# Performance work log

Hardware: AMD Instinct MI355X
Metric: run time of the kernel (lower is better)

Reference implementation:

```python
import jax, jax.numpy as jnp
import numpy as np

N, E = 10000, 100000
WIDTH, KER_WIDTH, DEPTH = 32, 128, 3
EDGE_ATTR_DIM, IN_WIDTH, OUT_WIDTH, COORD_DIM = 6, 3, 1, 3


def _glorot(k, fan_in, fan_out):
    return jax.random.normal(k, (fan_in, fan_out), jnp.float32) / np.sqrt(fan_in).astype(np.float32)


def setup_inputs() -> dict:
    key = jax.random.key(0)
    ks = jax.random.split(key, 16)
    z = lambda n: jnp.zeros((n,), jnp.float32)
    return {
        "x": jax.random.normal(ks[0], (N, IN_WIDTH), jnp.float32),
        "edge_index": jax.random.randint(ks[1], (2, E), 0, N),
        "edge_attr": jax.random.normal(ks[2], (E, EDGE_ATTR_DIM), jnp.float32),
        "coords_init": jax.random.normal(ks[3], (N, COORD_DIM), jnp.float32),
        "fc1_w": _glorot(ks[4], IN_WIDTH, WIDTH), "fc1_b": z(WIDTH),
        "ker_w1": _glorot(ks[5], EDGE_ATTR_DIM + 1, KER_WIDTH // 2), "ker_b1": z(KER_WIDTH // 2),
        "ker_w2": _glorot(ks[6], KER_WIDTH // 2, KER_WIDTH), "ker_b2": z(KER_WIDTH),
        "ker_w3": _glorot(ks[7], KER_WIDTH, WIDTH * WIDTH), "ker_b3": z(WIDTH * WIDTH),
        "cm_w1": _glorot(ks[8], WIDTH, WIDTH), "cm_b1": z(WIDTH),
        "cm_w2": _glorot(ks[9], WIDTH, 1) * 1e-3,  # xavier gain=0.001 coord head, no bias
        "fc2_w1": _glorot(ks[10], WIDTH, 2 * WIDTH), "fc2_b1": z(2 * WIDTH),
        "fc2_w2": _glorot(ks[11], 2 * WIDTH, OUT_WIDTH), "fc2_b2": z(OUT_WIDTH),
    }


def _seg_mean(data, seg, n):
    s = jax.ops.segment_sum(data, seg, num_segments=n)
    c = jax.ops.segment_sum(jnp.ones((seg.shape[0], 1), data.dtype), seg, num_segments=n)
    return s / jnp.clip(c, 1.0)


def reference(x, edge_index, edge_attr, coords_init,
              fc1_w, fc1_b, ker_w1, ker_b1, ker_w2, ker_b2, ker_w3, ker_b3,
              cm_w1, cm_b1, cm_w2, fc2_w1, fc2_b1, fc2_w2, fc2_b2):
    row, col = edge_index[0], edge_index[1]
    h = x @ fc1_w + fc1_b                                   # [N, W]
    coord = coords_init
    for _ in range(DEPTH):
        coord_diff = coord[row] - coord[col]                # [E, 3]
        radial = jnp.sum(coord_diff * coord_diff, axis=-1, keepdims=True)
        kin = jnp.concatenate([edge_attr, radial], axis=-1)  # [E, ker_in]
        k = jax.nn.relu(kin @ ker_w1 + ker_b1)
        k = jax.nn.relu(k @ ker_w2 + ker_b2)
        Wk = (k @ ker_w3 + ker_b3).reshape(E, WIDTH, WIDTH)  # per-edge kernel matrix
        m = jnp.einsum('eij,ej->ei', Wk, h[col])             # per-edge message [E, W]
        phi = jax.nn.relu(m @ cm_w1 + cm_b1) @ cm_w2         # [E, 1]
        coord = coord + _seg_mean(coord_diff * phi, row, N)  # equivariant coord update
        h = jax.nn.relu(h + _seg_mean(m, row, N))            # GKN node update
    out = jax.nn.relu(h @ fc2_w1 + fc2_b1) @ fc2_w2 + fc2_b2  # [N, out_width]
    return out, coord
```

## Files before the change

kernel.cpp:

```cpp
#include <hip/hip_runtime.h>
#include <hip/hip_bf16.h>

#define NN 10000
#define NE 100000

typedef __bf16 bf16x8 __attribute__((ext_vector_type(8)));
typedef float  f32x4  __attribute__((ext_vector_type(4)));
typedef unsigned int u32x4 __attribute__((ext_vector_type(4)));

__device__ __forceinline__ f32x4 relu4(f32x4 a) {
    a.x = fmaxf(a.x, 0.f); a.y = fmaxf(a.y, 0.f);
    a.z = fmaxf(a.z, 0.f); a.w = fmaxf(a.w, 0.f);
    return a;
}


__global__ void k_setup(const float* __restrict__ w3, __bf16* __restrict__ w3sw,
                        const float* __restrict__ w2, __bf16* __restrict__ w2sw,
                        const float* __restrict__ x, const float* __restrict__ fc1w,
                        const float* __restrict__ fc1b, const float* __restrict__ cinit,
                        float* __restrict__ h, float* __restrict__ coord,
                        const int* __restrict__ eidx, int* __restrict__ deg,
                        int* __restrict__ within) {
    int t = blockIdx.x * blockDim.x + threadIdx.x;
    if (t < 131072) {
        int jj = t & 7;
        int L  = (t >> 3) & 63;
        int ks = (t >> 9) & 3;
        int jt = (t >> 11) & 1;
        int i  = t >> 12;
        int c    = ks*32 + (L >> 4)*8 + jj;
        int colv = i*32 + jt*16 + (L & 15);
        w3sw[t] = (__bf16)w3[c*1024 + colv];
    } else if (t < 139264) {
        int u = t - 131072;
        int jj = u & 7;
        int L  = (u >> 3) & 63;
        int ks = (u >> 9) & 1;
        int nt = u >> 10;
        int c1 = ks*32 + (L >> 4)*8 + jj;
        int c2 = nt*16 + (L & 15);
        w2sw[u] = (__bf16)w2[c1*128 + c2];
    } else if (t < 139264 + NN) {
        int n = t - 139264;
        float x0 = x[n*3+0], x1 = x[n*3+1], x2 = x[n*3+2];
        #pragma unroll
        for (int j = 0; j < 32; j += 4) {
            f32x4 a = *(const f32x4*)(fc1b + j);
            a += x0 * (*(const f32x4*)(fc1w + 0*32 + j));
            a += x1 * (*(const f32x4*)(fc1w + 1*32 + j));
            a += x2 * (*(const f32x4*)(fc1w + 2*32 + j));
            *(f32x4*)(h + n*32 + j) = a;
        }
        coord[n*3+0] = cinit[n*3+0];
        coord[n*3+1] = cinit[n*3+1];
        coord[n*3+2] = cinit[n*3+2];
    } else if (t < 139264 + NN + NE) {
        int e = t - 139264 - NN;
        within[e] = atomicAdd(&deg[eidx[e]], 1);
    }
}

__global__ __launch_bounds__(1024, 1)
void k_scan(const int* __restrict__ deg, int* __restrict__ rowptr,
            float* __restrict__ deg_inv) {
    __shared__ int ssum[1024];
    const int tid = threadIdx.x;
    const int CH = 10;
    const int base = tid * CH;
    int s = 0;
    for (int i = 0; i < CH; ++i) { int n = base + i; if (n < NN) s += deg[n]; }
    ssum[tid] = s;
    __syncthreads();
    for (int off = 1; off < 1024; off <<= 1) {
        int t = (tid >= off) ? ssum[tid - off] : 0;
        __syncthreads();
        ssum[tid] += t;
        __syncthreads();
    }
    int run = ssum[tid] - s;
    for (int i = 0; i < CH; ++i) {
        int n = base + i;
        if (n < NN) {
            int d = deg[n];
            rowptr[n] = run; run += d;
            deg_inv[n] = 1.0f / (float)(d > 1 ? d : 1);
        }
    }
    if (tid == 1023) rowptr[NN] = ssum[1023];
}

__global__ __launch_bounds__(256, 2)
void k_layer(const float* __restrict__ coord, const int* __restrict__ eidx,
             const float* __restrict__ eattr,
             const float* __restrict__ w1, const float* __restrict__ b1,
             const __bf16* __restrict__ w2sw, const float* __restrict__ b2,
             const __bf16* __restrict__ w3sw, const float* __restrict__ b3,
             const float* __restrict__ h,
             const float* __restrict__ cm_w1, const float* __restrict__ cm_b1,
             const float* __restrict__ cm_w2,
             const int* __restrict__ rowptr, const int* __restrict__ within,
             float* __restrict__ cds, float* __restrict__ m_s,
             float* __restrict__ phis) {
    __shared__ unsigned smem_u[6656];
    __bf16* kt1 = (__bf16*)smem_u;
    __bf16* kt2 = (__bf16*)smem_u + 5120;
    const int lane = threadIdx.x & 63;
    const int wave = threadIdx.x >> 6;
    const int q = lane >> 4, t = lane & 15;
    const int base = blockIdx.x * 64;

    const int eg = base + lane;
    const int egc = eg < NE ? eg : NE - 1;
    const bool wvalid = eg < NE;
    const int r_node = eidx[egc];
    const int pos = rowptr[r_node] + within[egc];

    int col = eidx[NE + egc];
    float hcol[32];
    {
        const f32x4* hp = (const f32x4*)(h + (size_t)col * 32);
        #pragma unroll
        for (int v = 0; v < 8; ++v) {
            f32x4 hv = hp[v];
            hcol[v*4+0] = hv.x; hcol[v*4+1] = hv.y; hcol[v*4+2] = hv.z; hcol[v*4+3] = hv.w;
        }
    }
    bf16x8 bcur[8];
    {
        const __bf16* wb0 = w3sw + (size_t)(wave * 8) * 4096;
        #pragma unroll
        for (int f = 0; f < 8; ++f)
            bcur[f] = *(const bf16x8*)(wb0 + (f*64 + lane) * 8);
    }

    {
        float dx = coord[r_node*3+0] - coord[col*3+0];
        float dy = coord[r_node*3+1] - coord[col*3+1];
        float dz = coord[r_node*3+2] - coord[col*3+2];
        float rad = dx*dx + dy*dy + dz*dz;
        if (wave == 0 && wvalid) {
            f32x4 cdv = {dx, dy, dz, rad};
            *(f32x4*)(cds + (size_t)pos*4) = cdv;
        }
        float kin[7];
        #pragma unroll
        for (int a = 0; a < 6; ++a) kin[a] = eattr[(size_t)egc*6 + a];
        kin[6] = rad;

        const int g0 = wave * 16;
        f32x4 acc1[4];
        #pragma unroll
        for (int g = 0; g < 4; ++g) acc1[g] = *(const f32x4*)(b1 + g0 + g*4);
        #pragma unroll
        for (int t7 = 0; t7 < 7; ++t7) {
            float kv = kin[t7];
            #pragma unroll
            for (int g = 0; g < 4; ++g)
                acc1[g] += kv * (*(const f32x4*)(w1 + t7*64 + g0 + g*4));
        }
        #pragma unroll
        for (int cc = 0; cc < 2; ++cc) {
            f32x4 a0 = relu4(acc1[cc*2]), a1 = relu4(acc1[cc*2+1]);
            bf16x8 pk = {(__bf16)a0.x, (__bf16)a0.y, (__bf16)a0.z, (__bf16)a0.w,
                         (__bf16)a1.x, (__bf16)a1.y, (__bf16)a1.z, (__bf16)a1.w};
            int chunk = wave*2 + cc;
            *(bf16x8*)(kt1 + lane*72 + ((chunk ^ (lane & 7)) * 8)) = pk;
        }
    }
    __syncthreads();

    {
        bf16x8 af[4][2];
        #pragma unroll
        for (int mt = 0; mt < 4; ++mt) {
            int ep = mt*16 + t;
            #pragma unroll
            for (int ks = 0; ks < 2; ++ks)
                af[mt][ks] = *(const bf16x8*)(kt1 + ep*72 + (((ks*4 + q) ^ (ep & 7)) * 8));
        }
        #pragma unroll
        for (int nn = 0; nn < 2; ++nn) {
            int nt = wave*2 + nn;
            f32x4 a2[4];
            #pragma unroll
            for (int mt = 0; mt < 4; ++mt) a2[mt] = (f32x4){0.f, 0.f, 0.f, 0.f};
            #pragma unroll
            for (int ks = 0; ks < 2; ++ks) {
                bf16x8 bf_ = *(const bf16x8*)(w2sw + ((nt*2 + ks)*64 + lane) * 8);
                #pragma unroll
                for (int mt = 0; mt < 4; ++mt)
                    a2[mt] = __builtin_amdgcn_mfma_f32_16x16x32_bf16(af[mt][ks], bf_, a2[mt], 0, 0, 0);
            }
            float bias = b2[nt*16 + t];
            int chunk = nt*2 + (t >> 3);
            int tin = t & 7;
            #pragma unroll
            for (int mt = 0; mt < 4; ++mt) {
                #pragma unroll
                for (int rr = 0; rr < 4; ++rr) {
                    int row = mt*16 + q*4 + rr;
                    kt2[row*128 + ((chunk ^ (row & 15)) * 8) + tin] =
                        (__bf16)fmaxf(a2[mt][rr] + bias, 0.f);
                }
            }
        }
    }
    __syncthreads();

    bf16x8 afrag[4][4];
    #pragma unroll
    for (int mt = 0; mt < 4; ++mt) {
        int ep = mt*16 + t;
        #pragma unroll
        for (int ks = 0; ks < 4; ++ks) {
            int ck = ks*4 + q;
            afrag[mt][ks] = *(const bf16x8*)(kt2 + ep*128 + ((ck ^ (ep & 15)) * 8));
        }
    }
    __syncthreads();

    unsigned* wkw = smem_u + wave * 1280;
    const unsigned* wkrow = wkw + lane * 20;
    const int maskr = (lane ^ (lane >> 3)) & 3;
    float mv[8];

    #pragma unroll
    for (int ii = 0; ii < 8; ++ii) {
        const int i = wave * 8 + ii;
        f32x4 acc[4][2];
        #pragma unroll
        for (int mt = 0; mt < 4; ++mt) {
            acc[mt][0] = (f32x4){0.f, 0.f, 0.f, 0.f};
            acc[mt][1] = (f32x4){0.f, 0.f, 0.f, 0.f};
        }
        #pragma unroll
        for (int jt = 0; jt < 2; ++jt) {
            #pragma unroll
            for (int ks = 0; ks < 4; ++ks) {
                bf16x8 bfrag = bcur[jt*4 + ks];
                #pragma unroll
                for (int mt = 0; mt < 4; ++mt)
                    acc[mt][jt] = __builtin_amdgcn_mfma_f32_16x16x32_bf16(
                        afrag[mt][ks], bfrag, acc[mt][jt], 0, 0, 0);
            }
        }
        if (ii < 7) {
            const __bf16* wbn = w3sw + (size_t)(i + 1) * 4096;
            #pragma unroll
            for (int f = 0; f < 8; ++f)
                bcur[f] = *(const bf16x8*)(wbn + (f*64 + lane) * 8);
        }
        float bias0 = b3[i*32 + t];
        float bias1 = b3[i*32 + 16 + t];
        #pragma unroll
        for (int mt = 0; mt < 4; ++mt) {
            #pragma unroll
            for (int r = 0; r < 4; ++r) {
                int row = mt*16 + q*4 + r;
                float a0 = acc[mt][0][r] + bias0;
                float a1 = acc[mt][1][r] + bias1;
                unsigned u0 = (unsigned)__builtin_bit_cast(unsigned short, (__bf16)a0);
                unsigned u1 = (unsigned)__builtin_bit_cast(unsigned short, (__bf16)a1);
                int msk = (row ^ (row >> 3)) & 3;
                wkw[row*20 + ((((t >> 2) ^ msk) << 2) | (t & 3))] = u0 | (u1 << 16);
            }
        }
        float s = 0.f;
        #pragma unroll
        for (int j = 0; j < 4; ++j) {
            u32x4 wv = *(const u32x4*)(wkrow + ((j ^ maskr) << 2));
            #pragma unroll
            for (int k = 0; k < 4; ++k) {
                unsigned w = wv[k];
                int c = j*4 + k;
                float flo = __uint_as_float(w << 16);
                float fhi = __uint_as_float(w & 0xFFFF0000u);
                s += flo * hcol[c] + fhi * hcol[16 + c];
            }
        }
        mv[ii] = s;
    }

    if (wvalid) {
        f32x4 v0 = {mv[0], mv[1], mv[2], mv[3]};
        f32x4 v1 = {mv[4], mv[5], mv[6], mv[7]};
        *(f32x4*)(m_s + (size_t)pos*32 + wave*8)     = v0;
        *(f32x4*)(m_s + (size_t)pos*32 + wave*8 + 4) = v1;
    }

    __syncthreads();
    float* mvx = (float*)smem_u;
    #pragma unroll
    for (int ii = 0; ii < 8; ++ii)
        mvx[(wave*8 + ii)*65 + lane] = mv[ii];
    __syncthreads();
    if (wave == 0) {
        float m2[32];
        #pragma unroll
        for (int i = 0; i < 32; ++i) m2[i] = mvx[i*65 + lane];
        float phi = 0.f;
        for (int o = 0; o < 32; o += 4) {
            f32x4 a = *(const f32x4*)(cm_b1 + o);
            #pragma unroll
            for (int i = 0; i < 32; ++i)
                a += m2[i] * (*(const f32x4*)(cm_w1 + i*32 + o));
            a = relu4(a);
            f32x4 w2 = *(const f32x4*)(cm_w2 + o);
            phi += a.x*w2.x + a.y*w2.y + a.z*w2.z + a.w*w2.w;
        }
        if (wvalid) phis[pos] = phi;
    }
}

__global__ __launch_bounds__(256, 4)
void k_gather(const int* __restrict__ rowptr,
              const float* __restrict__ m_s, const float* __restrict__ phis,
              const float* __restrict__ cds, const float* __restrict__ deg_inv,
              float* __restrict__ coord, float* __restrict__ h,
              const float* __restrict__ fw1, const float* __restrict__ fb1,
              const float* __restrict__ fw2, const float* __restrict__ fb2,
              float* __restrict__ out, int dofinal) {
    int tid = blockIdx.x * blockDim.x + threadIdx.x;
    int n = tid >> 3, sub = tid & 7;
    if (n >= NN) return;
    int st = rowptr[n], en = rowptr[n+1];
    f32x4 am0 = {0.f, 0.f, 0.f, 0.f}, am1 = {0.f, 0.f, 0.f, 0.f};
    int p = st;
    for (; p + 1 < en; p += 2) {
        am0 += *(const f32x4*)(m_s + (size_t)p*32 + sub*4);
        am1 += *(const f32x4*)(m_s + (size_t)(p+1)*32 + sub*4);
    }
    if (p < en) am0 += *(const f32x4*)(m_s + (size_t)p*32 + sub*4);
    f32x4 am = am0 + am1;

    float di = deg_inv[n];
    f32x4 hv = *(const f32x4*)(h + (size_t)n*32 + sub*4);
    hv = relu4(hv + am * di);

    float c0 = 0.f, c1 = 0.f, c2 = 0.f;
    if (sub == 0) {
        float cx0 = 0.f, cy0 = 0.f, cz0 = 0.f;
        float cx1 = 0.f, cy1 = 0.f, cz1 = 0.f;
        int pp = st;
        for (; pp + 1 < en; pp += 2) {
            f32x4 cd0 = *(const f32x4*)(cds + (size_t)pp*4);
            f32x4 cd1 = *(const f32x4*)(cds + (size_t)(pp+1)*4);
            float p0 = phis[pp], p1 = phis[pp+1];
            cx0 += cd0.x * p0; cy0 += cd0.y * p0; cz0 += cd0.z * p0;
            cx1 += cd1.x * p1; cy1 += cd1.y * p1; cz1 += cd1.z * p1;
        }
        if (pp < en) {
            f32x4 cd0 = *(const f32x4*)(cds + (size_t)pp*4);
            float p0 = phis[pp];
            cx0 += cd0.x * p0; cy0 += cd0.y * p0; cz0 += cd0.z * p0;
        }
        c0 = coord[n*3+0] + (cx0 + cx1) * di;
        c1 = coord[n*3+1] + (cy0 + cy1) * di;
        c2 = coord[n*3+2] + (cz0 + cz1) * di;
    }

    if (!dofinal) {
        *(f32x4*)(h + (size_t)n*32 + sub*4) = hv;
        if (sub == 0) {
            coord[n*3+0] = c0; coord[n*3+1] = c1; coord[n*3+2] = c2;
        }
        return;
    }

    const int gbase = (tid & 63) & 56;
    float hreg[32];
    #pragma unroll
    for (int s2 = 0; s2 < 8; ++s2) {
        hreg[s2*4+0] = __shfl(hv.x, gbase + s2, 64);
        hreg[s2*4+1] = __shfl(hv.y, gbase + s2, 64);
        hreg[s2*4+2] = __shfl(hv.z, gbase + s2, 64);
        hreg[s2*4+3] = __shfl(hv.w, gbase + s2, 64);
    }
    float po = 0.f;
    #pragma unroll
    for (int oo = 0; oo < 8; oo += 4) {
        int o = sub*8 + oo;
        f32x4 a = *(const f32x4*)(fb1 + o);
        #pragma unroll
        for (int i = 0; i < 32; ++i)
            a += hreg[i] * (*(const f32x4*)(fw1 + i*64 + o));
        a = relu4(a);
        f32x4 w2 = *(const f32x4*)(fw2 + o);
        po += a.x*w2.x + a.y*w2.y + a.z*w2.z + a.w*w2.w;
    }
    po += __shfl_xor(po, 1, 64);
    po += __shfl_xor(po, 2, 64);
    po += __shfl_xor(po, 4, 64);
    if (sub == 0) {
        out[n] = po + fb2[0];
        out[NN + n*3 + 0] = c0;
        out[NN + n*3 + 1] = c1;
        out[NN + n*3 + 2] = c2;
    }
}


extern "C" void kernel_launch(void* const* d_in, const int* in_sizes, int n_in,
                              void* d_out, int out_size, void* d_ws, size_t ws_size,
                              hipStream_t stream) {
    const float* x      = (const float*)d_in[0];
    const int*   eidx   = (const int*)  d_in[1];
    const float* eattr  = (const float*)d_in[2];
    const float* cinit  = (const float*)d_in[3];
    const float* fc1w   = (const float*)d_in[4];
    const float* fc1b   = (const float*)d_in[5];
    const float* kw1    = (const float*)d_in[6];
    const float* kb1    = (const float*)d_in[7];
    const float* kw2    = (const float*)d_in[8];
    const float* kb2    = (const float*)d_in[9];
    const float* kw3    = (const float*)d_in[10];
    const float* kb3    = (const float*)d_in[11];
    const float* cmw1   = (const float*)d_in[12];
    const float* cmb1   = (const float*)d_in[13];
    const float* cmw2   = (const float*)d_in[14];
    const float* f2w1   = (const float*)d_in[15];
    const float* f2b1   = (const float*)d_in[16];
    const float* f2w2   = (const float*)d_in[17];
    const float* f2b2   = (const float*)d_in[18];
    float* out = (float*)d_out;

    char* p = (char*)d_ws;
    auto carve = [&](size_t bytes) {
        void* r = (void*)p;
        p += (bytes + 255) & ~(size_t)255;
        return r;
    };
    float*  h        = (float*) carve((size_t)NN * 32 * 4);
    float*  coord    = (float*) carve((size_t)NN * 3 * 4);
    int*    deg      = (int*)   carve((size_t)NN * 4);
    float*  deg_inv  = (float*) carve((size_t)NN * 4);
    int*    rowptr   = (int*)   carve((size_t)(NN + 1) * 4);
    int*    within   = (int*)   carve((size_t)NE * 4);
    float*  cds      = (float*) carve((size_t)NE * 4 * 4);
    float*  m_s      = (float*) carve((size_t)NE * 32 * 4);
    float*  phis     = (float*) carve((size_t)NE * 4);
    __bf16* w3sw     = (__bf16*)carve((size_t)131072 * 2);
    __bf16* w2sw     = (__bf16*)carve((size_t)8192 * 2);

    const int TB = 256;
    dim3 b(TB);
    dim3 gS((139264 + NN + NE + TB - 1) / TB);
    dim3 gG((NE + 63) / 64);
    dim3 gA((NN*8 + TB - 1) / TB);

    hipMemsetAsync(deg, 0, (size_t)NN * 4, stream);
    k_setup<<<gS, b, 0, stream>>>(kw3, w3sw, kw2, w2sw, x, fc1w, fc1b, cinit,
                                  h, coord, eidx, deg, within);
    k_scan <<<1, dim3(1024), 0, stream>>>(deg, rowptr, deg_inv);

    for (int d = 0; d < 3; ++d) {
        k_layer<<<gG, b, 0, stream>>>(coord, eidx, eattr, kw1, kb1, w2sw, kb2,
                                      w3sw, kb3, h, cmw1, cmb1, cmw2,
                                      rowptr, within, cds, m_s, phis);
        k_gather<<<gA, b, 0, stream>>>(rowptr, m_s, phis, cds, deg_inv, coord, h,
                                       f2w1, f2b1, f2w2, f2b2, out, d == 2 ? 1 : 0);
    }
}
```

Measured before the change: 332.8 us.

## Reassociate per-edge kernel matmul into per-node W3·h precompute with column-sorted edge segments

Rather than building each edge's full 32x32 kernel matrix and multiplying it by h[col], the code first computes a per-node tensor R[v] = W3 contracted with h[v] (plus a bias term) in a separate GEMM kernel. Edges are then grouped by source column into segments of 16, so one wave reuses R[col] for all its edges and needs only a small 128x32 MFMA per edge. The coord-MLP is also moved onto MFMA. This removes the dominant E×128×1024 GEMM at the cost of an NN×4096 bf16 intermediate written every layer, extra CSC setup kernels, and more bf16 rounding.

```diff
diff --git a/kernel.cpp b/kernel.cpp
--- a/kernel.cpp
+++ b/kernel.cpp
@@ -3,10 +3,10 @@
 
 #define NN 10000
 #define NE 100000
+#define NSEG_MAX 16384
 
 typedef __bf16 bf16x8 __attribute__((ext_vector_type(8)));
 typedef float  f32x4  __attribute__((ext_vector_type(4)));
-typedef unsigned int u32x4 __attribute__((ext_vector_type(4)));
 
 __device__ __forceinline__ f32x4 relu4(f32x4 a) {
     a.x = fmaxf(a.x, 0.f); a.y = fmaxf(a.y, 0.f);
@@ -14,35 +14,52 @@
     return a;
 }
 
-
-__global__ void k_setup(const float* __restrict__ w3, __bf16* __restrict__ w3sw,
-                        const float* __restrict__ w2, __bf16* __restrict__ w2sw,
+__device__ __forceinline__ unsigned pk2(float a, float b) {
+    unsigned ua = (unsigned)__builtin_bit_cast(unsigned short, (__bf16)a);
+    unsigned ub = (unsigned)__builtin_bit_cast(unsigned short, (__bf16)b);
+    return ua | (ub << 16);
+}
+
+__global__ void k_setup(const float* __restrict__ w3, __bf16* __restrict__ w3t_sw,
+                        const float* __restrict__ b3, __bf16* __restrict__ b3t_sw,
+                        const float* __restrict__ w2, __bf16* __restrict__ w2t_sw,
+                        const float* __restrict__ cw1, __bf16* __restrict__ cmw1_sw,
                         const float* __restrict__ x, const float* __restrict__ fc1w,
                         const float* __restrict__ fc1b, const float* __restrict__ cinit,
                         float* __restrict__ h, float* __restrict__ coord,
-                        const int* __restrict__ eidx, int* __restrict__ deg,
-                        int* __restrict__ within) {
+                        const int* __restrict__ eidx,
+                        int* __restrict__ deg, int* __restrict__ within,
+                        int* __restrict__ degc, int* __restrict__ withinc) {
     int t = blockIdx.x * blockDim.x + threadIdx.x;
     if (t < 131072) {
-        int jj = t & 7;
-        int L  = (t >> 3) & 63;
-        int ks = (t >> 9) & 3;
-        int jt = (t >> 11) & 1;
-        int i  = t >> 12;
-        int c    = ks*32 + (L >> 4)*8 + jj;
-        int colv = i*32 + jt*16 + (L & 15);
-        w3sw[t] = (__bf16)w3[c*1024 + colv];
-    } else if (t < 139264) {
-        int u = t - 131072;
-        int jj = u & 7;
-        int L  = (u >> 3) & 63;
-        int ks = (u >> 9) & 1;
-        int nt = u >> 10;
-        int c1 = ks*32 + (L >> 4)*8 + jj;
-        int c2 = nt*16 + (L & 15);
-        w2sw[u] = (__bf16)w2[c1*128 + c2];
-    } else if (t < 139264 + NN) {
-        int n = t - 139264;
+        int jj = t & 7, l = (t >> 3) & 63, ut = t >> 9;
+        int u  = ut*16 + (l & 15);
+        int j2 = ((l >> 4) & 3)*8 + jj;
+        int f  = u >> 9, ll = (u >> 3) & 63, j0 = u & 7;
+        int c  = (f & 3)*32 + ((ll >> 4) & 3)*8 + j0;
+        int i  = (f >> 2)*16 + (ll & 15);
+        w3t_sw[t] = (__bf16)w3[c*1024 + i*32 + j2];
+    } else if (t < 132096) {
+        int idx = t - 131072;
+        int jj = idx & 7, l = (idx >> 3) & 63, tt = idx >> 9;
+        int i  = tt*16 + (l & 15);
+        int j2 = ((l >> 4) & 3)*8 + jj;
+        b3t_sw[idx] = (__bf16)b3[i*32 + j2];
+    } else if (t < 140288) {
+        int idx = t - 132096;
+        int jj = idx & 7, l = (idx >> 3) & 63, g = idx >> 9;
+        int ct = g >> 1, ks = g & 1;
+        int c  = ct*16 + (l & 15);
+        int ch = ks*32 + ((l >> 4) & 3)*8 + jj;
+        w2t_sw[idx] = (__bf16)w2[ch*128 + c];
+    } else if (t < 142336) {
+        int idx = t - 140288;
+        int jj = idx & 7, l = (idx >> 3) & 63, ot = idx >> 9;
+        int o  = ot*16 + (l & 15);
+        int i  = ((l >> 4) & 3)*8 + jj;
+        cmw1_sw[idx] = (__bf16)cw1[i*32 + o];
+    } else if (t < 142336 + NN) {
+        int n = t - 142336;
         float x0 = x[n*3+0], x1 = x[n*3+1], x2 = x[n*3+2];
         #pragma unroll
         for (int j = 0; j < 32; j += 4) {
@@ -55,28 +72,32 @@
         coord[n*3+0] = cinit[n*3+0];
         coord[n*3+1] = cinit[n*3+1];
         coord[n*3+2] = cinit[n*3+2];
-    } else if (t < 139264 + NN + NE) {
-        int e = t - 139264 - NN;
+    } else if (t < 142336 + NN + NE) {
+        int e = t - 142336 - NN;
         within[e] = atomicAdd(&deg[eidx[e]], 1);
+    } else if (t < 142336 + NN + 2*NE) {
+        int e = t - 142336 - NN - NE;
+        withinc[e] = atomicAdd(&degc[eidx[NE + e]], 1);
     }
 }
 
 __global__ __launch_bounds__(1024, 1)
 void k_scan(const int* __restrict__ deg, int* __restrict__ rowptr,
-            float* __restrict__ deg_inv) {
+            float* __restrict__ deg_inv,
+            const int* __restrict__ degc, int* __restrict__ colptr,
+            int* __restrict__ seg_meta, int* __restrict__ seg_start) {
     __shared__ int ssum[1024];
     const int tid = threadIdx.x;
     const int CH = 10;
     const int base = tid * CH;
+
     int s = 0;
     for (int i = 0; i < CH; ++i) { int n = base + i; if (n < NN) s += deg[n]; }
     ssum[tid] = s;
     __syncthreads();
     for (int off = 1; off < 1024; off <<= 1) {
         int t = (tid >= off) ? ssum[tid - off] : 0;
-        __syncthreads();
-        ssum[tid] += t;
-        __syncthreads();
+        __syncthreads(); ssum[tid] += t; __syncthreads();
     }
     int run = ssum[tid] - s;
     for (int i = 0; i < CH; ++i) {
@@ -88,228 +109,247 @@
         }
     }
     if (tid == 1023) rowptr[NN] = ssum[1023];
-}
-
-__global__ __launch_bounds__(256, 2)
-void k_layer(const float* __restrict__ coord, const int* __restrict__ eidx,
-             const float* __restrict__ eattr,
-             const float* __restrict__ w1, const float* __restrict__ b1,
-             const __bf16* __restrict__ w2sw, const float* __restrict__ b2,
-             const __bf16* __restrict__ w3sw, const float* __restrict__ b3,
-             const float* __restrict__ h,
-             const float* __restrict__ cm_w1, const float* __restrict__ cm_b1,
-             const float* __restrict__ cm_w2,
-             const int* __restrict__ rowptr, const int* __restrict__ within,
-             float* __restrict__ cds, float* __restrict__ m_s,
-             float* __restrict__ phis) {
-    __shared__ unsigned smem_u[6656];
-    __bf16* kt1 = (__bf16*)smem_u;
-    __bf16* kt2 = (__bf16*)smem_u + 5120;
+    __syncthreads();
+
+    s = 0;
+    for (int i = 0; i < CH; ++i) { int n = base + i; if (n < NN) s += degc[n]; }
+    ssum[tid] = s;
+    __syncthreads();
+    for (int off = 1; off < 1024; off <<= 1) {
+        int t = (tid >= off) ? ssum[tid - off] : 0;
+        __syncthreads(); ssum[tid] += t; __syncthreads();
+    }
+    run = ssum[tid] - s;
+    for (int i = 0; i < CH; ++i) {
+        int n = base + i;
+        if (n < NN) { colptr[n] = run; run += degc[n]; }
+    }
+    if (tid == 1023) colptr[NN] = ssum[1023];
+    __syncthreads();
+
+    s = 0;
+    for (int i = 0; i < CH; ++i) { int n = base + i; if (n < NN) s += (degc[n] + 15) >> 4; }
+    ssum[tid] = s;
+    __syncthreads();
+    for (int off = 1; off < 1024; off <<= 1) {
+        int t = (tid >= off) ? ssum[tid - off] : 0;
+        __syncthreads(); ssum[tid] += t; __syncthreads();
+    }
+    run = ssum[tid] - s;
+    for (int i = 0; i < CH; ++i) {
+        int n = base + i;
+        if (n < NN) {
+            int d = degc[n], ns = (d + 15) >> 4, cp = colptr[n];
+            for (int k = 0; k < ns; ++k) {
+                int cnt = d - k*16; if (cnt > 16) cnt = 16;
+                seg_meta[run + k]  = n | (cnt << 16);
+                seg_start[run + k] = cp + k*16;
+            }
+            run += ns;
+        }
+    }
+    __syncthreads();
+    int nseg = ssum[1023];
+    for (int sg = nseg + tid; sg < NSEG_MAX; sg += 1024) seg_meta[sg] = -1;
+}
+
+__global__ void k_setup2(const int* __restrict__ eidx, const float* __restrict__ eattr,
+                         const int* __restrict__ rowptr, const int* __restrict__ within,
+                         const int* __restrict__ colptr, const int* __restrict__ withinc,
+                         int* __restrict__ cs_pos, int* __restrict__ cs_row,
+                         float* __restrict__ eattr_cs) {
+    int e = blockIdx.x * blockDim.x + threadIdx.x;
+    if (e >= NE) return;
+    int row = eidx[e], col = eidx[NE + e];
+    int pos = rowptr[row] + within[e];
+    int cs  = colptr[col] + withinc[e];
+    cs_pos[cs] = pos; cs_row[cs] = row;
+    #pragma unroll
+    for (int a = 0; a < 6; ++a) eattr_cs[(size_t)cs*8 + a] = eattr[(size_t)e*6 + a];
+    eattr_cs[(size_t)cs*8 + 6] = 0.f; eattr_cs[(size_t)cs*8 + 7] = 0.f;
+}
+
+
+__global__ __launch_bounds__(256, 4)
+void k_rgemm(const float* __restrict__ h, const __bf16* __restrict__ w3t_sw,
+             const __bf16* __restrict__ b3t_sw,
+             __bf16* __restrict__ r_sw, float* __restrict__ bt) {
     const int lane = threadIdx.x & 63;
-    const int wave = threadIdx.x >> 6;
-    const int q = lane >> 4, t = lane & 15;
-    const int base = blockIdx.x * 64;
-
-    const int eg = base + lane;
-    const int egc = eg < NE ? eg : NE - 1;
-    const bool wvalid = eg < NE;
-    const int r_node = eidx[egc];
-    const int pos = rowptr[r_node] + within[egc];
-
-    int col = eidx[NE + egc];
-    float hcol[32];
-    {
-        const f32x4* hp = (const f32x4*)(h + (size_t)col * 32);
-        #pragma unroll
-        for (int v = 0; v < 8; ++v) {
-            f32x4 hv = hp[v];
-            hcol[v*4+0] = hv.x; hcol[v*4+1] = hv.y; hcol[v*4+2] = hv.z; hcol[v*4+3] = hv.w;
-        }
-    }
-    bf16x8 bcur[8];
-    {
-        const __bf16* wb0 = w3sw + (size_t)(wave * 8) * 4096;
-        #pragma unroll
-        for (int f = 0; f < 8; ++f)
-            bcur[f] = *(const bf16x8*)(wb0 + (f*64 + lane) * 8);
-    }
-
-    {
-        float dx = coord[r_node*3+0] - coord[col*3+0];
-        float dy = coord[r_node*3+1] - coord[col*3+1];
-        float dz = coord[r_node*3+2] - coord[col*3+2];
-        float rad = dx*dx + dy*dy + dz*dz;
-        if (wave == 0 && wvalid) {
+    const int q = lane >> 4;
+    const int job = blockIdx.x * 4 + (threadIdx.x >> 6);
+    const int vt = job >> 2, uq = job & 3;
+    const int v = vt*16 + (lane & 15);
+
+    f32x4 h0 = *(const f32x4*)(h + (size_t)v*32 + q*8);
+    f32x4 h1 = *(const f32x4*)(h + (size_t)v*32 + q*8 + 4);
+    bf16x8 bfrag;
+    bfrag[0]=(__bf16)h0.x; bfrag[1]=(__bf16)h0.y; bfrag[2]=(__bf16)h0.z; bfrag[3]=(__bf16)h0.w;
+    bfrag[4]=(__bf16)h1.x; bfrag[5]=(__bf16)h1.y; bfrag[6]=(__bf16)h1.z; bfrag[7]=(__bf16)h1.w;
+
+    const f32x4 zero = {0.f, 0.f, 0.f, 0.f};
+    const int ut0 = uq * 64;
+    #pragma unroll 8
+    for (int g = 0; g < 64; ++g) {
+        int ut = ut0 + g;
+        bf16x8 af = *(const bf16x8*)(w3t_sw + ((size_t)ut*64 + lane)*8);
+        f32x4 c = __builtin_amdgcn_mfma_f32_16x16x32_bf16(af, bfrag, zero, 0, 0, 0);
+        uint2 pv = { pk2(c.x, c.y), pk2(c.z, c.w) };
+        *(uint2*)(r_sw + (size_t)v*4096 + ut*16 + q*4) = pv;
+    }
+    if (uq == 0) {
+        #pragma unroll
+        for (int tt = 0; tt < 2; ++tt) {
+            bf16x8 af = *(const bf16x8*)(b3t_sw + ((size_t)tt*64 + lane)*8);
+            f32x4 c = __builtin_amdgcn_mfma_f32_16x16x32_bf16(af, bfrag, zero, 0, 0, 0);
+            *(f32x4*)(bt + (size_t)v*32 + tt*16 + q*4) = c;
+        }
+    }
+}
+
+__global__ __launch_bounds__(256, 3)
+void k_edge(const int* __restrict__ seg_meta, const int* __restrict__ seg_start,
+            const int* __restrict__ cs_pos, const int* __restrict__ cs_row,
+            const float* __restrict__ eattr_cs, const float* __restrict__ coord,
+            const float* __restrict__ w1, const float* __restrict__ b1,
+            const __bf16* __restrict__ w2t_sw, const float* __restrict__ b2,
+            const __bf16* __restrict__ r_sw, const float* __restrict__ bt,
+            const __bf16* __restrict__ cmw1_sw, const float* __restrict__ cm_b1,
+            const float* __restrict__ cm_w2,
+            float* __restrict__ cds, float* __restrict__ m_s,
+            float* __restrict__ phis) {
+    const int lane = threadIdx.x & 63;
+    const int q  = lane >> 4;
+    const int el = lane & 15;
+    const int sid = blockIdx.x * 4 + (threadIdx.x >> 6);
+    const int meta = seg_meta[sid];
+    if (meta < 0) return;
+    const int v     = meta & 0xFFFF;
+    const int cnt   = meta >> 16;
+    const int start = seg_start[sid];
+
+    bf16x8 rA[8];
+    #pragma unroll
+    for (int f = 0; f < 8; ++f)
+        rA[f] = *(const bf16x8*)(r_sw + (size_t)v*4096 + (f*64 + lane)*8);
+    f32x4 btv0 = *(const f32x4*)(bt + (size_t)v*32 + q*4);
+    f32x4 btv1 = *(const f32x4*)(bt + (size_t)v*32 + 16 + q*4);
+
+    int slot = start + el; if (slot >= NE) slot = NE - 1;
+    const int pos   = cs_pos[slot];
+    const int rnode = cs_row[slot];
+
+    const float dx = coord[rnode*3+0] - coord[v*3+0];
+    const float dy = coord[rnode*3+1] - coord[v*3+1];
+    const float dz = coord[rnode*3+2] - coord[v*3+2];
+    const float rad = dx*dx + dy*dy + dz*dz;
+
+    f32x4 ea0 = *(const f32x4*)(eattr_cs + (size_t)slot*8);
+    f32x4 ea1 = *(const f32x4*)(eattr_cs + (size_t)slot*8 + 4);
+    const float kin[7] = {ea0.x, ea0.y, ea0.z, ea0.w, ea1.x, ea1.y, rad};
+
+    bf16x8 k1f[2];
+    #pragma unroll
+    for (int ks = 0; ks < 2; ++ks) {
+        const int c0 = ks*32 + q*8;
+        f32x4 a0 = *(const f32x4*)(b1 + c0);
+        f32x4 a1 = *(const f32x4*)(b1 + c0 + 4);
+        #pragma unroll
+        for (int a = 0; a < 7; ++a) {
+            const float kv = kin[a];
+            a0 += kv * (*(const f32x4*)(w1 + a*64 + c0));
+            a1 += kv * (*(const f32x4*)(w1 + a*64 + c0 + 4));
+        }
+        a0 = relu4(a0); a1 = relu4(a1);
+        bf16x8 t;
+        t[0]=(__bf16)a0.x; t[1]=(__bf16)a0.y; t[2]=(__bf16)a0.z; t[3]=(__bf16)a0.w;
+        t[4]=(__bf16)a1.x; t[5]=(__bf16)a1.y; t[6]=(__bf16)a1.z; t[7]=(__bf16)a1.w;
+        k1f[ks] = t;
+    }
+
+    const f32x4 zero = {0.f, 0.f, 0.f, 0.f};
+    f32x4 C2[8];
+    #pragma unroll
+    for (int ct = 0; ct < 8; ++ct) {
+        f32x4 acc = zero;
+        #pragma unroll
+        for (int ks = 0; ks < 2; ++ks) {
+            bf16x8 af = *(const bf16x8*)(w2t_sw + ((ct*2 + ks)*64 + lane)*8);
+            acc = __builtin_amdgcn_mfma_f32_16x16x32_bf16(af, k1f[ks], acc, 0, 0, 0);
+        }
+        f32x4 bb = *(const f32x4*)(b2 + ct*16 + q*4);
+        C2[ct] = relu4(acc + bb);
+    }
+
+    const int lowq = q & 1, hiq = q >> 1;
+    bf16x8 k2f[4];
+    #pragma unroll
+    for (int ks2 = 0; ks2 < 4; ++ks2) {
+        bf16x8 t;
+        #pragma unroll
+        for (int hh = 0; hh < 2; ++hh) {
+            const int src = (lowq*2 + hh)*16 + el;
+            #pragma unroll
+            for (int rr = 0; rr < 4; ++rr) {
+                const float x0 = __shfl(C2[ks2*2][rr],     src, 64);
+                const float x1 = __shfl(C2[ks2*2 + 1][rr], src, 64);
+                t[hh*4 + rr] = (__bf16)(hiq ? x1 : x0);
+            }
+        }
+        k2f[ks2] = t;
+    }
+
+    f32x4 M0 = zero, M1 = zero;
+    #pragma unroll
+    for (int ks2 = 0; ks2 < 4; ++ks2) {
+        M0 = __builtin_amdgcn_mfma_f32_16x16x32_bf16(rA[ks2],     k2f[ks2], M0, 0, 0, 0);
+        M1 = __builtin_amdgcn_mfma_f32_16x16x32_bf16(rA[4 + ks2], k2f[ks2], M1, 0, 0, 0);
+    }
+    M0 += btv0; M1 += btv1;
+
+    const bool ev = el < cnt;
+    if (ev) {
+        *(f32x4*)(m_s + (size_t)pos*32 + q*4)      = M0;
+        *(f32x4*)(m_s + (size_t)pos*32 + 16 + q*4) = M1;
+        if (q == 0) {
             f32x4 cdv = {dx, dy, dz, rad};
             *(f32x4*)(cds + (size_t)pos*4) = cdv;
         }
-        float kin[7];
-        #pragma unroll
-        for (int a = 0; a < 6; ++a) kin[a] = eattr[(size_t)egc*6 + a];
-        kin[6] = rad;
-
-        const int g0 = wave * 16;
-        f32x4 acc1[4];
-        #pragma unroll
-        for (int g = 0; g < 4; ++g) acc1[g] = *(const f32x4*)(b1 + g0 + g*4);
-        #pragma unroll
-        for (int t7 = 0; t7 < 7; ++t7) {
-            float kv = kin[t7];
-            #pragma unroll
-            for (int g = 0; g < 4; ++g)
-                acc1[g] += kv * (*(const f32x4*)(w1 + t7*64 + g0 + g*4));
-        }
-        #pragma unroll
-        for (int cc = 0; cc < 2; ++cc) {
-            f32x4 a0 = relu4(acc1[cc*2]), a1 = relu4(acc1[cc*2+1]);
-            bf16x8 pk = {(__bf16)a0.x, (__bf16)a0.y, (__bf16)a0.z, (__bf16)a0.w,
-                         (__bf16)a1.x, (__bf16)a1.y, (__bf16)a1.z, (__bf16)a1.w};
-            int chunk = wave*2 + cc;
-            *(bf16x8*)(kt1 + lane*72 + ((chunk ^ (lane & 7)) * 8)) = pk;
-        }
-    }
-    __syncthreads();
-
-    {
-        bf16x8 af[4][2];
-        #pragma unroll
-        for (int mt = 0; mt < 4; ++mt) {
-            int ep = mt*16 + t;
-            #pragma unroll
-            for (int ks = 0; ks < 2; ++ks)
-                af[mt][ks] = *(const bf16x8*)(kt1 + ep*72 + (((ks*4 + q) ^ (ep & 7)) * 8));
-        }
-        #pragma unroll
-        for (int nn = 0; nn < 2; ++nn) {
-            int nt = wave*2 + nn;
-            f32x4 a2[4];
-            #pragma unroll
-            for (int mt = 0; mt < 4; ++mt) a2[mt] = (f32x4){0.f, 0.f, 0.f, 0.f};
-            #pragma unroll
-            for (int ks = 0; ks < 2; ++ks) {
-                bf16x8 bf_ = *(const bf16x8*)(w2sw + ((nt*2 + ks)*64 + lane) * 8);
-                #pragma unroll
-                for (int mt = 0; mt < 4; ++mt)
-                    a2[mt] = __builtin_amdgcn_mfma_f32_16x16x32_bf16(af[mt][ks], bf_, a2[mt], 0, 0, 0);
-            }
-            float bias = b2[nt*16 + t];
-            int chunk = nt*2 + (t >> 3);
-            int tin = t & 7;
-            #pragma unroll
-            for (int mt = 0; mt < 4; ++mt) {
-                #pragma unroll
-                for (int rr = 0; rr < 4; ++rr) {
-                    int row = mt*16 + q*4 + rr;
-                    kt2[row*128 + ((chunk ^ (row & 15)) * 8) + tin] =
-                        (__bf16)fmaxf(a2[mt][rr] + bias, 0.f);
-                }
-            }
-        }
-    }
-    __syncthreads();
-
-    bf16x8 afrag[4][4];
-    #pragma unroll
-    for (int mt = 0; mt < 4; ++mt) {
-        int ep = mt*16 + t;
-        #pragma unroll
-        for (int ks = 0; ks < 4; ++ks) {
-            int ck = ks*4 + q;
-            afrag[mt][ks] = *(const bf16x8*)(kt2 + ep*128 + ((ck ^ (ep & 15)) * 8));
-        }
-    }
-    __syncthreads();
-
-    unsigned* wkw = smem_u + wave * 1280;
-    const unsigned* wkrow = wkw + lane * 20;
-    const int maskr = (lane ^ (lane >> 3)) & 3;
-    float mv[8];
-
-    #pragma unroll
-    for (int ii = 0; ii < 8; ++ii) {
-        const int i = wave * 8 + ii;
-        f32x4 acc[4][2];
-        #pragma unroll
-        for (int mt = 0; mt < 4; ++mt) {
-            acc[mt][0] = (f32x4){0.f, 0.f, 0.f, 0.f};
-            acc[mt][1] = (f32x4){0.f, 0.f, 0.f, 0.f};
-        }
-        #pragma unroll
-        for (int jt = 0; jt < 2; ++jt) {
-            #pragma unroll
-            for (int ks = 0; ks < 4; ++ks) {
-                bf16x8 bfrag = bcur[jt*4 + ks];
-                #pragma unroll
-                for (int mt = 0; mt < 4; ++mt)
-                    acc[mt][jt] = __builtin_amdgcn_mfma_f32_16x16x32_bf16(
-                        afrag[mt][ks], bfrag, acc[mt][jt], 0, 0, 0);
-            }
-        }
-        if (ii < 7) {
-            const __bf16* wbn = w3sw + (size_t)(i + 1) * 4096;
-            #pragma unroll
-            for (int f = 0; f < 8; ++f)
-                bcur[f] = *(const bf16x8*)(wbn + (f*64 + lane) * 8);
-        }
-        float bias0 = b3[i*32 + t];
-        float bias1 = b3[i*32 + 16 + t];
-        #pragma unroll
-        for (int mt = 0; mt < 4; ++mt) {
-            #pragma unroll
-            for (int r = 0; r < 4; ++r) {
-                int row = mt*16 + q*4 + r;
-                float a0 = acc[mt][0][r] + bias0;
-                float a1 = acc[mt][1][r] + bias1;
-                unsigned u0 = (unsigned)__builtin_bit_cast(unsigned short, (__bf16)a0);
-                unsigned u1 = (unsigned)__builtin_bit_cast(unsigned short, (__bf16)a1);
-                int msk = (row ^ (row >> 3)) & 3;
-                wkw[row*20 + ((((t >> 2) ^ msk) << 2) | (t & 3))] = u0 | (u1 << 16);
-            }
-        }
-        float s = 0.f;
-        #pragma unroll
-        for (int j = 0; j < 4; ++j) {
-            u32x4 wv = *(const u32x4*)(wkrow + ((j ^ maskr) << 2));
-            #pragma unroll
-            for (int k = 0; k < 4; ++k) {
-                unsigned w = wv[k];
-                int c = j*4 + k;
-                float flo = __uint_as_float(w << 16);
-                float fhi = __uint_as_float(w & 0xFFFF0000u);
-                s += flo * hcol[c] + fhi * hcol[16 + c];
-            }
-        }
-        mv[ii] = s;
-    }
-
-    if (wvalid) {
-        f32x4 v0 = {mv[0], mv[1], mv[2], mv[3]};
-        f32x4 v1 = {mv[4], mv[5], mv[6], mv[7]};
-        *(f32x4*)(m_s + (size_t)pos*32 + wave*8)     = v0;
-        *(f32x4*)(m_s + (size_t)pos*32 + wave*8 + 4) = v1;
-    }
-
-    __syncthreads();
-    float* mvx = (float*)smem_u;
-    #pragma unroll
-    for (int ii = 0; ii < 8; ++ii)
-        mvx[(wave*8 + ii)*65 + lane] = mv[ii];
-    __syncthreads();
-    if (wave == 0) {
-        float m2[32];
-        #pragma unroll
-        for (int i = 0; i < 32; ++i) m2[i] = mvx[i*65 + lane];
-        float phi = 0.f;
-        for (int o = 0; o < 32; o += 4) {
-            f32x4 a = *(const f32x4*)(cm_b1 + o);
-            #pragma unroll
-            for (int i = 0; i < 32; ++i)
-                a += m2[i] * (*(const f32x4*)(cm_w1 + i*32 + o));
-            a = relu4(a);
-            f32x4 w2 = *(const f32x4*)(cm_w2 + o);
-            phi += a.x*w2.x + a.y*w2.y + a.z*w2.z + a.w*w2.w;
-        }
-        if (wvalid) phis[pos] = phi;
+    }
+
+    bf16x8 paf;
+    #pragma unroll
+    for (int hh = 0; hh < 2; ++hh) {
+        const int src = (lowq*2 + hh)*16 + el;
+        #pragma unroll
+        for (int rr = 0; rr < 4; ++rr) {
+            const float x0 = __shfl(M0[rr], src, 64);
+            const float x1 = __shfl(M1[rr], src, 64);
+            paf[hh*4 + rr] = (__bf16)(hiq ? x1 : x0);
+        }
+    }
+    bf16x8 bf0 = *(const bf16x8*)(cmw1_sw + (0*64 + lane)*8);
+    bf16x8 bf1 = *(const bf16x8*)(cmw1_sw + (1*64 + lane)*8);
+    f32x4 PH0 = __builtin_amdgcn_mfma_f32_16x16x32_bf16(paf, bf0, zero, 0, 0, 0);
+    f32x4 PH1 = __builtin_amdgcn_mfma_f32_16x16x32_bf16(paf, bf1, zero, 0, 0, 0);
+
+    const float b1v0 = cm_b1[el], b1v1 = cm_b1[16 + el];
+    const float w2v0 = cm_w2[el], w2v1 = cm_w2[16 + el];
+    float ph[4]; int pr[4];
+    #pragma unroll
+    for (int r = 0; r < 4; ++r) {
+        float s0 = fmaxf(PH0[r] + b1v0, 0.f) * w2v0
+                 + fmaxf(PH1[r] + b1v1, 0.f) * w2v1;
+        s0 += __shfl_xor(s0, 1, 64);
+        s0 += __shfl_xor(s0, 2, 64);
+        s0 += __shfl_xor(s0, 4, 64);
+        s0 += __shfl_xor(s0, 8, 64);
+        ph[r] = s0;
+        pr[r] = __shfl(pos, (q << 4) + q*4 + r, 64);
+    }
+    if (el == 0) {
+        #pragma unroll
+        for (int r = 0; r < 4; ++r)
+            if (q*4 + r < cnt) phis[pr[r]] = ph[r];
     }
 }
 
@@ -437,27 +477,48 @@
     float*  deg_inv  = (float*) carve((size_t)NN * 4);
     int*    rowptr   = (int*)   carve((size_t)(NN + 1) * 4);
     int*    within   = (int*)   carve((size_t)NE * 4);
+    int*    degc     = (int*)   carve((size_t)NN * 4);
+    int*    colptr   = (int*)   carve((size_t)(NN + 1) * 4);
+    int*    withinc  = (int*)   carve((size_t)NE * 4);
+    int*    cs_pos   = (int*)   carve((size_t)NE * 4);
+    int*    cs_row   = (int*)   carve((size_t)NE * 4);
+    float*  eattr_cs = (float*) carve((size_t)NE * 8 * 4);
+    int*    seg_meta = (int*)   carve((size_t)NSEG_MAX * 4);
+    int*    seg_start= (int*)   carve((size_t)NSEG_MAX * 4);
     float*  cds      = (float*) carve((size_t)NE * 4 * 4);
     float*  m_s      = (float*) carve((size_t)NE * 32 * 4);
     float*  phis     = (float*) carve((size_t)NE * 4);
-    __bf16* w3sw     = (__bf16*)carve((size_t)131072 * 2);
-    __bf16* w2sw     = (__bf16*)carve((size_t)8192 * 2);
+    float*  bt       = (float*) carve((size_t)NN * 32 * 4);
+    __bf16* w3t_sw   = (__bf16*)carve((size_t)131072 * 2);
+    __bf16* b3t_sw   = (__bf16*)carve((size_t)1024 * 2);
+    __bf16* w2t_sw   = (__bf16*)carve((size_t)8192 * 2);
+    __bf16* cmw1_sw  = (__bf16*)carve((size_t)2048 * 2);
+    __bf16* r_sw     = (__bf16*)carve((size_t)NN * 4096 * 2);
 
     const int TB = 256;
     dim3 b(TB);
-    dim3 gS((139264 + NN + NE + TB - 1) / TB);
-    dim3 gG((NE + 63) / 64);
+    const int totS = 142336 + NN + 2*NE;
+    dim3 gS((totS + TB - 1) / TB);
+    dim3 gS2((NE + TB - 1) / TB);
+    dim3 gR(625);
+    dim3 gE(NSEG_MAX / 4);
     dim3 gA((NN*8 + TB - 1) / TB);
 
     hipMemsetAsync(deg, 0, (size_t)NN * 4, stream);
-    k_setup<<<gS, b, 0, stream>>>(kw3, w3sw, kw2, w2sw, x, fc1w, fc1b, cinit,
-                                  h, coord, eidx, deg, within);
-    k_scan <<<1, dim3(1024), 0, stream>>>(deg, rowptr, deg_inv);
+    hipMemsetAsync(degc, 0, (size_t)NN * 4, stream);
+    k_setup<<<gS, b, 0, stream>>>(kw3, w3t_sw, kb3, b3t_sw, kw2, w2t_sw, cmw1, cmw1_sw,
+                                  x, fc1w, fc1b, cinit, h, coord, eidx,
+                                  deg, within, degc, withinc);
+    k_scan<<<1, dim3(1024), 0, stream>>>(deg, rowptr, deg_inv, degc, colptr,
+                                         seg_meta, seg_start);
+    k_setup2<<<gS2, b, 0, stream>>>(eidx, eattr, rowptr, within, colptr, withinc,
+                                    cs_pos, cs_row, eattr_cs);
 
     for (int d = 0; d < 3; ++d) {
-        k_layer<<<gG, b, 0, stream>>>(coord, eidx, eattr, kw1, kb1, w2sw, kb2,
-                                      w3sw, kb3, h, cmw1, cmb1, cmw2,
-                                      rowptr, within, cds, m_s, phis);
+        k_rgemm<<<gR, b, 0, stream>>>(h, w3t_sw, b3t_sw, r_sw, bt);
+        k_edge<<<gE, b, 0, stream>>>(seg_meta, seg_start, cs_pos, cs_row, eattr_cs,
+                                     coord, kw1, kb1, w2t_sw, kb2, r_sw, bt,
+                                     cmw1_sw, cmb1, cmw2, cds, m_s, phis);
         k_gather<<<gA, b, 0, stream>>>(rowptr, m_s, phis, cds, deg_inv, coord, h,
                                        f2w1, f2b1, f2w2, f2b2, out, d == 2 ? 1 : 0);
     }
```

Result: slower. 385.6 us (+15.9%).
